# Optimization experiments

Measured on AMD Instinct MI355X. Metric: run time of the kernel, lower is better.

The kernel has to match this reference:

```python
import jax, jax.numpy as jnp
import numpy as np


def setup_inputs() -> dict:
    key = jax.random.key(0)
    ks = jax.random.split(key, 8)
    B, T, U = 4, 400, 80
    De, Dd, V = 512, 512, 1024
    F = De + Dd  # in_features = 1024
    s = lambda k, shape: jax.random.normal(k, shape, dtype=jnp.float32) * 0.05
    return {
        "encoder_output": jax.random.normal(ks[0], (B, T, De), dtype=jnp.float32),
        "decoder_output": jax.random.normal(ks[1], (B, U, Dd), dtype=jnp.float32),
        "W_enc": s(ks[2], (F, De)),
        "b_enc": s(ks[3], (F,)),
        "W_dec": s(ks[4], (F, Dd)),
        "b_dec": s(ks[5], (F,)),
        "W_fc": s(ks[6], (V, F)),
        "b_fc": s(ks[7], (V,)),
    }


def reference(encoder_output, decoder_output, W_enc, b_enc, W_dec, b_dec, W_fc, b_fc):
    # fc_enc / fc_dec projections: (B,T,F) and (B,U,F)
    enc = jnp.einsum("btd,fd->btf", encoder_output, W_enc) + b_enc
    dec = jnp.einsum("bud,fd->buf", decoder_output, W_dec) + b_dec
    # broadcast-add -> (B,T,U,F)
    combined = enc[:, :, None, :] + dec[:, None, :, :]
    # fc: tanh then linear -> (B,T,U,V)
    vocab_logits = jnp.einsum("btuf,vf->btuv", jnp.tanh(combined), W_fc) + b_fc
    # HAT branch: blank prob via sigmoid of logit 0
    blk_logit = vocab_logits[..., :1]
    log_blk = jax.nn.log_sigmoid(blk_logit)          # log(sigmoid)
    log_not_blk = jax.nn.log_sigmoid(-blk_logit)     # log(1 - sigmoid)
    vocab_log_probs = log_not_blk + jax.nn.log_softmax(vocab_logits[..., 1:], axis=-1)
    return jnp.concatenate([log_blk, vocab_log_probs], axis=-1)
```

## Files before the change

kernel.cpp:

```cpp
#include <hip/hip_runtime.h>
#include <hip/hip_bf16.h>
#include <cstdint>
#include <cstddef>

typedef short bf16x8 __attribute__((ext_vector_type(8)));
typedef float f32x4 __attribute__((ext_vector_type(4)));

static __device__ __forceinline__ unsigned short f2bf(float f) {
    union { float f; uint32_t u; } c; c.f = f;
    uint32_t r = c.u + 0x7FFFu + ((c.u >> 16) & 1u);
    return (unsigned short)(r >> 16);
}
static __device__ __forceinline__ float bf2f_lo(uint32_t w) {
    union { uint32_t u; float f; } c; c.u = w << 16; return c.f;
}
static __device__ __forceinline__ float bf2f_hi(uint32_t w) {
    union { uint32_t u; float f; } c; c.u = w & 0xffff0000u; return c.f;
}
static __device__ __forceinline__ float fast_tanh(float x) {
    float e = __expf(2.0f * x);
    return 1.0f - 2.0f / (e + 1.0f);
}
static __device__ __forceinline__ float softplus_f(float x) {
    return fmaxf(x, 0.0f) + log1pf(__expf(-fabsf(x)));
}

#define GLOAD_LDS16(g, l) \
    __builtin_amdgcn_global_load_lds((const __attribute__((address_space(1))) void*)(g), \
                                     (__attribute__((address_space(3))) void*)(l), 16, 0, 0)

__global__ __launch_bounds__(256) void k_convert(
    const float* __restrict__ s0, const float* __restrict__ s1,
    const float* __restrict__ s2, const float* __restrict__ s3,
    const float* __restrict__ s4,
    unsigned short* __restrict__ d0, unsigned short* __restrict__ d1,
    unsigned short* __restrict__ d2, unsigned short* __restrict__ d3,
    unsigned short* __restrict__ d4,
    int n0, int n1, int n2, int n3, int n4)
{
    int i = blockIdx.x * 256 + threadIdx.x;
    int c0 = n0 >> 2, c1 = c0 + (n1 >> 2), c2 = c1 + (n2 >> 2),
        c3 = c2 + (n3 >> 2), c4 = c3 + (n4 >> 2);
    if (i >= c4) return;
    const float* s; unsigned short* d; int j;
    if (i < c0)      { s = s0; d = d0; j = i; }
    else if (i < c1) { s = s1; d = d1; j = i - c0; }
    else if (i < c2) { s = s2; d = d2; j = i - c1; }
    else if (i < c3) { s = s3; d = d3; j = i - c2; }
    else             { s = s4; d = d4; j = i - c3; }
    float4 v = reinterpret_cast<const float4*>(s)[j];
    ushort4 o;
    o.x = f2bf(v.x); o.y = f2bf(v.y); o.z = f2bf(v.z); o.w = f2bf(v.w);
    reinterpret_cast<ushort4*>(d)[j] = o;
}

__global__ __launch_bounds__(256) void k_proj(
    const unsigned short* __restrict__ A,
    const unsigned short* __restrict__ W,
    const float* __restrict__ bias,
    float* __restrict__ out)
{
    __shared__ unsigned short As[32 * 512];
    const int tid = threadIdx.x;
    const int m0 = blockIdx.x * 32;
    const int c0 = blockIdx.y * 128;
    {
        int row = tid >> 3;
        const unsigned short* src = A + (size_t)(m0 + row) * 512;
        unsigned int base = row * 1024;
        unsigned int sw = (row & 7) << 4;
        #pragma unroll
        for (int c = 0; c < 8; ++c) {
            int col = (tid & 7) * 8 + c * 64;
            bf16x8 v = *reinterpret_cast<const bf16x8*>(src + col);
            *reinterpret_cast<bf16x8*>(
                reinterpret_cast<char*>(As) + ((base + col * 2) ^ sw)) = v;
        }
    }
    __syncthreads();
    const int w = tid >> 6, l = tid & 63;
    const int lr = l & 15, lkb = (l >> 4) * 8;
    f32x4 acc[2][2] = {};
    const int colbase = c0 + w * 32;
    const unsigned short* Wb = W + (size_t)(colbase + lr) * 512 + lkb;
    const unsigned int sw = (lr & 7) << 4;
    for (int ks = 0; ks < 16; ++ks) {
        unsigned int kb = (ks * 32 + lkb) * 2;
        bf16x8 a0 = *reinterpret_cast<const bf16x8*>(
            reinterpret_cast<const char*>(As) + ((lr * 1024 + kb) ^ sw));
        bf16x8 a1 = *reinterpret_cast<const bf16x8*>(
            reinterpret_cast<const char*>(As) + (((16 + lr) * 1024 + kb) ^ sw));
        #pragma unroll
        for (int nf = 0; nf < 2; ++nf) {
            bf16x8 b = *reinterpret_cast<const bf16x8*>(Wb + nf * 16 * 512 + ks * 32);
            acc[0][nf] = __builtin_amdgcn_mfma_f32_16x16x32_bf16(a0, b, acc[0][nf], 0, 0, 0);
            acc[1][nf] = __builtin_amdgcn_mfma_f32_16x16x32_bf16(a1, b, acc[1][nf], 0, 0, 0);
        }
    }
    const int qr = (l >> 4) * 4;
    #pragma unroll
    for (int nf = 0; nf < 2; ++nf) {
        int col = colbase + nf * 16 + lr;
        float bv = bias[col];
        #pragma unroll
        for (int mf = 0; mf < 2; ++mf)
            #pragma unroll
            for (int r = 0; r < 4; ++r)
                out[(size_t)(m0 + mf * 16 + qr + r) * 1024 + col] = acc[mf][nf][r] + bv;
    }
}

__global__ __launch_bounds__(256) void k_tanhA(
    const float* __restrict__ enc_f,
    const float* __restrict__ dec_f,
    char* __restrict__ outb)
{
    const int NG = 128000 * 128;
    for (int g = blockIdx.x * 256 + threadIdx.x; g < NG; g += gridDim.x * 256) {
        int row = g >> 7, c8 = g & 127;
        int bt = row / 80;
        int u = row - bt * 80;
        int b = bt / 400;
        const float* ep = enc_f + (size_t)bt * 1024 + c8 * 8;
        const float* dp = dec_f + (size_t)(b * 80 + u) * 1024 + c8 * 8;
        float4 e0 = *(const float4*)ep, e1 = *(const float4*)(ep + 4);
        float4 f0 = *(const float4*)dp, f1 = *(const float4*)(dp + 4);
        uint4 pk;
        pk.x = (uint32_t)f2bf(fast_tanh(e0.x + f0.x)) | ((uint32_t)f2bf(fast_tanh(e0.y + f0.y)) << 16);
        pk.y = (uint32_t)f2bf(fast_tanh(e0.z + f0.z)) | ((uint32_t)f2bf(fast_tanh(e0.w + f0.w)) << 16);
        pk.z = (uint32_t)f2bf(fast_tanh(e1.x + f1.x)) | ((uint32_t)f2bf(fast_tanh(e1.y + f1.y)) << 16);
        pk.w = (uint32_t)f2bf(fast_tanh(e1.z + f1.z)) | ((uint32_t)f2bf(fast_tanh(e1.w + f1.w)) << 16);
        *(uint4*)(outb + (size_t)row * 4096 + c8 * 16) = pk;
    }
}

__global__ __launch_bounds__(256, 4) void k_gemm(
    const unsigned short* __restrict__ Wfc,
    const float* __restrict__ bfc,
    char* __restrict__ outb)
{
    __shared__ char As[16384];
    __shared__ char Bs[16384];
    const int tid = threadIdx.x;
    const int w = tid >> 6, l = tid & 63;
    const int lr = l & 15, q = l >> 4;
    const int wm = w >> 1, wn = w & 1;

    const int bid = (int)blockIdx.x;
    const int xcd = bid & 7, loc = bid >> 3;
    const size_t R0 = (size_t)(xcd * 125 + (loc >> 3)) * 128;
    const int n0 = (loc & 7) * 128;

    const char* srcA[4]; const char* srcB[4];
    unsigned dst[4];
    #pragma unroll
    for (int i = 0; i < 4; ++i) {
        unsigned d = tid * 16 + i * 4096;
        unsigned L = d ^ (((d >> 7) & 7u) << 4);
        unsigned row = L >> 7, kb = L & 127u;
        dst[i] = d;
        srcA[i] = outb + (R0 + row) * 4096 + kb;
        srcB[i] = (const char*)Wfc + (size_t)(n0 + row) * 2048 + kb;
    }

    const unsigned key = (unsigned)((lr & 7) << 4);
    unsigned aoff[4], boff[4];
    #pragma unroll
    for (int mf = 0; mf < 4; ++mf) aoff[mf] = (unsigned)((wm * 64 + mf * 16 + lr) * 128);
    #pragma unroll
    for (int nf = 0; nf < 4; ++nf) boff[nf] = (unsigned)((wn * 64 + nf * 16 + lr) * 128);

    f32x4 acc[4][4] = {};

    for (int ks = 0; ks < 16; ++ks) {
        #pragma unroll
        for (int i = 0; i < 4; ++i) {
            GLOAD_LDS16(srcA[i] + ks * 128, As + dst[i]);
            GLOAD_LDS16(srcB[i] + ks * 128, Bs + dst[i]);
        }
        __syncthreads();
        #pragma unroll
        for (int kk = 0; kk < 2; ++kk) {
            const unsigned ko = (unsigned)(kk * 64 + q * 16) ^ key;
            bf16x8 af[4], bf[4];
            #pragma unroll
            for (int mf = 0; mf < 4; ++mf) af[mf] = *(const bf16x8*)(As + aoff[mf] + ko);
            #pragma unroll
            for (int nf = 0; nf < 4; ++nf) bf[nf] = *(const bf16x8*)(Bs + boff[nf] + ko);
            #pragma unroll
            for (int nf = 0; nf < 4; ++nf)
                #pragma unroll
                for (int mf = 0; mf < 4; ++mf)
                    acc[nf][mf] = __builtin_amdgcn_mfma_f32_16x16x32_bf16(
                        bf[nf], af[mf], acc[nf][mf], 0, 0, 0);
        }
        __syncthreads();
    }

    const int vq = n0 + wn * 64 + q * 4;
    #pragma unroll
    for (int nf = 0; nf < 4; ++nf) {
        float4 bv = *(const float4*)(bfc + vq + nf * 16);
        #pragma unroll
        for (int mf = 0; mf < 4; ++mf) {
            f32x4 v = acc[nf][mf];
            uint2 pk;
            pk.x = (uint32_t)f2bf(v[0] + bv.x) | ((uint32_t)f2bf(v[1] + bv.y) << 16);
            pk.y = (uint32_t)f2bf(v[2] + bv.z) | ((uint32_t)f2bf(v[3] + bv.w) << 16);
            size_t m = R0 + (size_t)(wm * 64 + mf * 16 + lr);
            *(uint2*)(outb + m * 4096 + 2048 + (size_t)(vq + nf * 16) * 2) = pk;
        }
    }
}

__global__ __launch_bounds__(256) void k_softmax(char* __restrict__ outb)
{
    const int row = blockIdx.x * 4 + (threadIdx.x >> 6);
    const int l = threadIdx.x & 63;
    const char* lp = outb + (size_t)row * 4096 + 2048 + l * 32;
    uint4 wa = *(const uint4*)lp;
    uint4 wb = *(const uint4*)(lp + 16);
    float v[16];
    uint32_t wd[8] = { wa.x, wa.y, wa.z, wa.w, wb.x, wb.y, wb.z, wb.w };
    #pragma unroll
    for (int i = 0; i < 8; ++i) { v[2*i] = bf2f_lo(wd[i]); v[2*i+1] = bf2f_hi(wd[i]); }

    float l0 = __shfl(v[0], 0);
    float m = (l == 0) ? -3.0e38f : v[0];
    #pragma unroll
    for (int i = 1; i < 16; ++i) m = fmaxf(m, v[i]);
    #pragma unroll
    for (int s = 1; s < 64; s <<= 1) m = fmaxf(m, __shfl_xor(m, s));
    float s = (l == 0) ? 0.0f : __expf(v[0] - m);
    #pragma unroll
    for (int i = 1; i < 16; ++i) s += __expf(v[i] - m);
    #pragma unroll
    for (int sh = 1; sh < 64; sh <<= 1) s += __shfl_xor(s, sh);

    float lse = m + __logf(s);
    float fin = -lse - softplus_f(l0);
    float f0v = -softplus_f(-l0);

    float* op = (float*)(outb + (size_t)row * 4096) + l * 16;
    #pragma unroll
    for (int c = 0; c < 4; ++c) {
        float4 o;
        o.x = v[4*c+0] + fin; o.y = v[4*c+1] + fin;
        o.z = v[4*c+2] + fin; o.w = v[4*c+3] + fin;
        if (l == 0 && c == 0) o.x = f0v;
        *(float4*)(op + 4*c) = o;
    }
}

extern "C" void kernel_launch(void* const* d_in, const int* in_sizes, int n_in,
                              void* d_out, int out_size, void* d_ws, size_t ws_size,
                              hipStream_t stream)
{
    const float* encoder = (const float*)d_in[0];
    const float* decoder = (const float*)d_in[1];
    const float* W_enc   = (const float*)d_in[2];
    const float* b_enc   = (const float*)d_in[3];
    const float* W_dec   = (const float*)d_in[4];
    const float* b_dec   = (const float*)d_in[5];
    const float* W_fc    = (const float*)d_in[6];
    const float* b_fc    = (const float*)d_in[7];
    char* outb = (char*)d_out;

    char* ws = (char*)d_ws;
    float*          enc_f  = (float*)(ws);
    float*          dec_f  = (float*)(ws + 6553600);
    unsigned short* Wfc_h  = (unsigned short*)(ws + 7864320);
    unsigned short* Wenc_h = (unsigned short*)(ws + 9961472);
    unsigned short* Wdec_h = (unsigned short*)(ws + 11010048);
    unsigned short* encI_h = (unsigned short*)(ws + 12058624);
    unsigned short* decI_h = (unsigned short*)(ws + 13697024);

    const int nEnc = 4 * 400 * 512, nDec = 4 * 80 * 512;
    const int nWe = 1024 * 512, nWd = 1024 * 512, nWf = 1024 * 1024;
    const int totalF4 = (nEnc + nDec + nWe + nWd + nWf) >> 2;
    k_convert<<<(totalF4 + 255) / 256, 256, 0, stream>>>(
        encoder, decoder, W_enc, W_dec, W_fc,
        encI_h, decI_h, Wenc_h, Wdec_h, Wfc_h,
        nEnc, nDec, nWe, nWd, nWf);

    k_proj<<<dim3(1600 / 32, 8), 256, 0, stream>>>(encI_h, Wenc_h, b_enc, enc_f);
    k_proj<<<dim3(320 / 32, 8), 256, 0, stream>>>(decI_h, Wdec_h, b_dec, dec_f);

    k_tanhA<<<4096, 256, 0, stream>>>(enc_f, dec_f, outb);
    k_gemm<<<8000, 256, 0, stream>>>(Wfc_h, b_fc, outb);
    k_softmax<<<32000, 256, 0, stream>>>(outb);
}
```

Before: 688.4 us.

## Restructure vocab GEMM into 256x256 tiles with double-buffered LDS pipeline

The main logits GEMM moves from 128x128 tiles with 4 waves and single-buffered LDS to 256x256 tiles with 8 waves and 128KB of dynamic LDS split into two buffers. The next K slice's global-to-LDS loads are issued while the current slice is computed. Compute is split into barrier-interleaved quarters with raised wave priority around the MFMA bursts. This aims to raise data reuse per tile and hide load latency, at the cost of one block per CU and higher register pressure (128 accumulator floats per thread).

```diff
diff --git a/kernel.cpp b/kernel.cpp
--- a/kernel.cpp
+++ b/kernel.cpp
@@ -134,81 +134,119 @@
     }
 }
 
-__global__ __launch_bounds__(256, 4) void k_gemm(
+__global__ __launch_bounds__(512, 1) void k_gemm(
     const unsigned short* __restrict__ Wfc,
     const float* __restrict__ bfc,
     char* __restrict__ outb)
 {
-    __shared__ char As[16384];
-    __shared__ char Bs[16384];
+    extern __shared__ char smem[];
     const int tid = threadIdx.x;
     const int w = tid >> 6, l = tid & 63;
     const int lr = l & 15, q = l >> 4;
-    const int wm = w >> 1, wn = w & 1;
+    const int wm = w >> 2, wn = w & 3;
 
     const int bid = (int)blockIdx.x;
-    const int xcd = bid & 7, loc = bid >> 3;
-    const size_t R0 = (size_t)(xcd * 125 + (loc >> 3)) * 128;
-    const int n0 = (loc & 7) * 128;
-
-    const char* srcA[4]; const char* srcB[4];
-    unsigned dst[4];
-    #pragma unroll
-    for (int i = 0; i < 4; ++i) {
-        unsigned d = tid * 16 + i * 4096;
-        unsigned L = d ^ (((d >> 7) & 7u) << 4);
-        unsigned row = L >> 7, kb = L & 127u;
-        dst[i] = d;
-        srcA[i] = outb + (R0 + row) * 4096 + kb;
-        srcB[i] = (const char*)Wfc + (size_t)(n0 + row) * 2048 + kb;
-    }
+    const int g = (bid & 7) * 250 + (bid >> 3);
+    const size_t R0 = (size_t)(g >> 2) * 256;
+    const int n0 = (g & 3) * 256;
+
+    const unsigned kb0 = (unsigned)(((tid & 7) * 16) ^ (((tid >> 3) & 7) << 4));
+    const int row0 = tid >> 3;
+    const char* sA = outb + (R0 + row0) * 4096 + kb0;
+    const char* sB = (const char*)Wfc + (size_t)(n0 + row0) * 2048 + kb0;
+
+#define STAGE(dbuf, koff) do { \
+    const char* _a = sA + (koff); \
+    const char* _b = sB + (koff); \
+    char* _d = smem + (dbuf) * 65536 + tid * 16; \
+    GLOAD_LDS16(_a,          _d);          \
+    GLOAD_LDS16(_a + 262144, _d + 8192);   \
+    GLOAD_LDS16(_a + 524288, _d + 16384);  \
+    GLOAD_LDS16(_a + 786432, _d + 24576);  \
+    GLOAD_LDS16(_b,          _d + 32768);  \
+    GLOAD_LDS16(_b + 131072, _d + 40960);  \
+    GLOAD_LDS16(_b + 262144, _d + 49152);  \
+    GLOAD_LDS16(_b + 393216, _d + 57344);  \
+} while (0)
 
     const unsigned key = (unsigned)((lr & 7) << 4);
-    unsigned aoff[4], boff[4];
-    #pragma unroll
-    for (int mf = 0; mf < 4; ++mf) aoff[mf] = (unsigned)((wm * 64 + mf * 16 + lr) * 128);
-    #pragma unroll
-    for (int nf = 0; nf < 4; ++nf) boff[nf] = (unsigned)((wn * 64 + nf * 16 + lr) * 128);
-
-    f32x4 acc[4][4] = {};
-
-    for (int ks = 0; ks < 16; ++ks) {
+    const unsigned kx0 = (unsigned)(q * 16) ^ key;
+    const unsigned kx1 = (unsigned)(q * 16 + 64) ^ key;
+    const unsigned abase = (unsigned)((wm * 128 + lr) * 128);
+    const unsigned bbase = (unsigned)(32768 + (wn * 64 + lr) * 128);
+
+    f32x4 acc[8][4] = {};
+    bf16x8 af[4][2], bf[4][2];
+
+    STAGE(0, 0);
+    asm volatile("s_waitcnt vmcnt(0)" ::: "memory");
+    __builtin_amdgcn_s_barrier();
+    __builtin_amdgcn_sched_barrier(0);
+
+#define LDA(h) do { \
+    _Pragma("unroll") \
+    for (int mf = 0; mf < 4; ++mf) { \
+        const char* _p = smem + cb + abase + (h) * 8192 + mf * 2048; \
+        af[mf][0] = *(const bf16x8*)(_p + kx0); \
+        af[mf][1] = *(const bf16x8*)(_p + kx1); \
+    } } while (0)
+#define LDB(gg) do { \
+    _Pragma("unroll") \
+    for (int j = 0; j < 2; ++j) { \
+        const char* _p = smem + cb + bbase + ((gg) * 2 + j) * 2048; \
+        bf[(gg) * 2 + j][0] = *(const bf16x8*)(_p + kx0); \
+        bf[(gg) * 2 + j][1] = *(const bf16x8*)(_p + kx1); \
+    } } while (0)
+#define MFQ(h, gg) do { \
+    __builtin_amdgcn_s_setprio(1); \
+    _Pragma("unroll") \
+    for (int j = 0; j < 2; ++j) \
+        _Pragma("unroll") \
+        for (int ks = 0; ks < 2; ++ks) \
+            _Pragma("unroll") \
+            for (int mf = 0; mf < 4; ++mf) \
+                acc[(h) * 4 + mf][(gg) * 2 + j] = __builtin_amdgcn_mfma_f32_16x16x32_bf16( \
+                    bf[(gg) * 2 + j][ks], af[mf][ks], acc[(h) * 4 + mf][(gg) * 2 + j], 0, 0, 0); \
+    __builtin_amdgcn_s_setprio(0); \
+} while (0)
+
+    #pragma unroll 2
+    for (int t = 0; t < 16; ++t) {
+        const unsigned cb = (unsigned)(t & 1) * 65536;
+        if (t + 1 < 16) STAGE((t & 1) ^ 1, (t + 1) * 128);
+        LDA(0);
+        LDB(0);
+        __builtin_amdgcn_s_barrier();
+        MFQ(0, 0);
+        LDB(1);
+        __builtin_amdgcn_s_barrier();
+        MFQ(0, 1);
+        LDA(1);
+        __builtin_amdgcn_s_barrier();
+        MFQ(1, 1);
+        __builtin_amdgcn_s_barrier();
+        MFQ(1, 0);
+        asm volatile("s_waitcnt vmcnt(0)" ::: "memory");
+        __builtin_amdgcn_s_barrier();
+        __builtin_amdgcn_sched_barrier(0);
+    }
+#undef LDA
+#undef LDB
+#undef MFQ
+#undef STAGE
+
+    #pragma unroll
+    for (int nf = 0; nf < 4; ++nf) {
+        const int v = n0 + wn * 64 + nf * 16 + q * 4;
+        float4 bv = *(const float4*)(bfc + v);
         #pragma unroll
-        for (int i = 0; i < 4; ++i) {
-            GLOAD_LDS16(srcA[i] + ks * 128, As + dst[i]);
-            GLOAD_LDS16(srcB[i] + ks * 128, Bs + dst[i]);
-        }
-        __syncthreads();
-        #pragma unroll
-        for (int kk = 0; kk < 2; ++kk) {
-            const unsigned ko = (unsigned)(kk * 64 + q * 16) ^ key;
-            bf16x8 af[4], bf[4];
-            #pragma unroll
-            for (int mf = 0; mf < 4; ++mf) af[mf] = *(const bf16x8*)(As + aoff[mf] + ko);
-            #pragma unroll
-            for (int nf = 0; nf < 4; ++nf) bf[nf] = *(const bf16x8*)(Bs + boff[nf] + ko);
-            #pragma unroll
-            for (int nf = 0; nf < 4; ++nf)
-                #pragma unroll
-                for (int mf = 0; mf < 4; ++mf)
-                    acc[nf][mf] = __builtin_amdgcn_mfma_f32_16x16x32_bf16(
-                        bf[nf], af[mf], acc[nf][mf], 0, 0, 0);
-        }
-        __syncthreads();
-    }
-
-    const int vq = n0 + wn * 64 + q * 4;
-    #pragma unroll
-    for (int nf = 0; nf < 4; ++nf) {
-        float4 bv = *(const float4*)(bfc + vq + nf * 16);
-        #pragma unroll
-        for (int mf = 0; mf < 4; ++mf) {
-            f32x4 v = acc[nf][mf];
+        for (int mf8 = 0; mf8 < 8; ++mf8) {
+            f32x4 a = acc[mf8][nf];
             uint2 pk;
-            pk.x = (uint32_t)f2bf(v[0] + bv.x) | ((uint32_t)f2bf(v[1] + bv.y) << 16);
-            pk.y = (uint32_t)f2bf(v[2] + bv.z) | ((uint32_t)f2bf(v[3] + bv.w) << 16);
-            size_t m = R0 + (size_t)(wm * 64 + mf * 16 + lr);
-            *(uint2*)(outb + m * 4096 + 2048 + (size_t)(vq + nf * 16) * 2) = pk;
+            pk.x = (uint32_t)f2bf(a[0] + bv.x) | ((uint32_t)f2bf(a[1] + bv.y) << 16);
+            pk.y = (uint32_t)f2bf(a[2] + bv.z) | ((uint32_t)f2bf(a[3] + bv.w) << 16);
+            size_t m = R0 + (size_t)(wm * 128 + mf8 * 16 + lr);
+            *(uint2*)(outb + m * 4096 + 2048 + (size_t)v * 2) = pk;
         }
     }
 }
@@ -287,6 +325,11 @@
     k_proj<<<dim3(320 / 32, 8), 256, 0, stream>>>(decI_h, Wdec_h, b_dec, dec_f);
 
     k_tanhA<<<4096, 256, 0, stream>>>(enc_f, dec_f, outb);
-    k_gemm<<<8000, 256, 0, stream>>>(Wfc_h, b_fc, outb);
+
+    const int GEMM_SMEM = 131072;
+    hipFuncSetAttribute(reinterpret_cast<const void*>(k_gemm),
+                        hipFuncAttributeMaxDynamicSharedMemorySize, GEMM_SMEM);
+    k_gemm<<<2000, 512, GEMM_SMEM, stream>>>(Wfc_h, b_fc, outb);
+
     k_softmax<<<32000, 256, 0, stream>>>(outb);
 }
```

New measurement: 697.4 us. No clear change (+1.3%).
